# Performance work log

Hardware: AMD Instinct MI355X
Metric: run time of the kernel (lower is better)

The kernel has to match this reference:

```python
import jax, jax.numpy as jnp
import numpy as np

D_MODEL = 256; D_STATE = 128; EXPAND = 2; HEADDIM = 64
D_INNER = EXPAND * D_MODEL            # 512
NHEADS = D_INNER // HEADDIM           # 8
CONV_DIM = D_INNER + 2 * D_STATE      # 768
D_IN_PROJ = 2 * D_INNER + 2 * D_STATE + NHEADS  # 1288
KCONV = 4
BATCH = 16; SEQ = 1024; CHUNK = 64
EPS = 1e-5


def setup_inputs() -> dict:
    key = jax.random.key(0)
    ks = jax.random.split(key, 8)
    # dt_bias = inverse-softplus of dt ~ U[1e-3, 1e-1] (Mamba2 init)
    dt = jnp.exp(jax.random.uniform(ks[3], (NHEADS,), jnp.float32,
                                    np.log(1e-3), np.log(1e-1)))
    dt_bias = dt + jnp.log(-jnp.expm1(-dt))
    return {
        "u": jax.random.normal(ks[0], (BATCH, SEQ, D_MODEL), jnp.float32),
        "W_in": 0.02 * jax.random.normal(ks[1], (D_MODEL, D_IN_PROJ), jnp.float32),
        "conv_w": 0.2 * jax.random.normal(ks[2], (CONV_DIM, KCONV), jnp.float32),
        "conv_b": jnp.zeros((CONV_DIM,), jnp.float32),
        "dt_bias": dt_bias,
        "A_log": jnp.log(jax.random.uniform(ks[4], (NHEADS,), jnp.float32, 1.0, 16.0)),
        "D": jnp.ones((NHEADS,), jnp.float32),
        "norm_w": jnp.ones((D_INNER,), jnp.float32),
        "W_out": 0.02 * jax.random.normal(ks[5], (D_INNER, D_MODEL), jnp.float32),
    }


def _segsum(x):
    # x: (..., L) -> (..., L, L) lower-triangular cumulative segment sums
    L = x.shape[-1]
    c = jnp.cumsum(x, axis=-1)
    ss = c[..., :, None] - c[..., None, :]
    mask = jnp.tril(jnp.ones((L, L), bool))
    return jnp.where(mask, ss, -jnp.inf)


def _ssd(X, A, Bm, Cm, chunk):
    # Chunked SSD selective scan (Mamba2, ngroups=1).
    # X:(b,t,h,p)  A:(b,t,h)  Bm,Cm:(b,t,n)
    b, t, h, p = X.shape
    nc = t // chunk
    X = X.reshape(b, nc, chunk, h, p)
    A = A.reshape(b, nc, chunk, h).transpose(0, 3, 1, 2)   # (b,h,c,l)
    Bm = Bm.reshape(b, nc, chunk, -1)
    Cm = Cm.reshape(b, nc, chunk, -1)
    A_cs = jnp.cumsum(A, axis=-1)                          # (b,h,c,l)
    Lmat = jnp.exp(_segsum(A))                             # (b,h,c,l,l)
    # within-chunk (diagonal) contribution
    Y_diag = jnp.einsum('bcln,bcsn,bhcls,bcshp->bclhp', Cm, Bm, Lmat, X)
    # per-chunk end states
    decay_states = jnp.exp(A_cs[..., -1:] - A_cs)          # (b,h,c,l)
    states = jnp.einsum('bcln,bhcl,bclhp->bchpn', Bm, decay_states, X)
    # inter-chunk recurrence (vectorized over chunks)
    A_chunk = jnp.pad(A_cs[..., -1], ((0, 0), (0, 0), (1, 0)))
    decay_chunk = jnp.exp(_segsum(A_chunk))                # (b,h,c+1,c+1)
    states = jnp.concatenate([jnp.zeros_like(states[:, :1]), states], axis=1)
    new_states = jnp.einsum('bhzc,bchpn->bzhpn', decay_chunk, states)
    states = new_states[:, :-1]                            # state entering each chunk
    Y_off = jnp.einsum('bcln,bchpn,bhcl->bclhp', Cm, states, jnp.exp(A_cs))
    return (Y_diag + Y_off).reshape(b, t, h, p)


def reference(u, W_in, conv_w, conv_b, dt_bias, A_log, D, norm_w, W_out):
    B, T, _ = u.shape
    zxbcdt = u @ W_in                                      # (B,T,1288)
    z, xBC, dt = jnp.split(zxbcdt, [D_INNER, D_INNER + CONV_DIM], axis=-1)
    # causal depthwise conv1d, kernel KCONV
    xp = jnp.pad(xBC, ((0, 0), (KCONV - 1, 0), (0, 0)))
    kern = conv_w.T[:, None, :]                            # (K,1,C)
    xBC = jax.lax.conv_general_dilated(
        xp, kern, (1,), 'VALID',
        dimension_numbers=('NWC', 'WIO', 'NWC'), feature_group_count=CONV_DIM)
    xBC = jax.nn.silu(xBC + conv_b)
    x, Bc, Cc = jnp.split(xBC, [D_INNER, D_INNER + D_STATE], axis=-1)
    x = x.reshape(B, T, NHEADS, HEADDIM)
    dt = jax.nn.softplus(dt + dt_bias)                     # (B,T,H)
    A = -jnp.exp(A_log)                                    # (H,)
    y = _ssd(x * dt[..., None], dt * A, Bc, Cc, CHUNK)     # (B,T,H,P)
    y = y + D[:, None] * x                                 # skip term
    y = y.reshape(B, T, D_INNER)
    # gated RMSNorm: norm(y * silu(z)) * weight
    g = y * jax.nn.silu(z)
    g = g * jax.lax.rsqrt(jnp.mean(g * g, axis=-1, keepdims=True) + EPS) * norm_w
    return g @ W_out
```

## Files before the change

kernel.cpp:

```cpp
#include <hip/hip_runtime.h>
#include <hip/hip_bf16.h>
#include <math.h>

#define BATCHN  16
#define SEQ     1024
#define DMODEL  256
#define DSTATE  128
#define HEADDIM 64
#define DINNER  512
#define NHEADS  8
#define CONVDIM 768
#define DINPROJ 1288
#define ZXLD    1280
#define KCONV   4
#define NCHUNK  16
#define LCHUNK  64
#define EPSV    1e-5f
#define ROWS    (BATCHN*SEQ)

typedef __attribute__((ext_vector_type(8))) __bf16 bf16x8;
typedef __attribute__((ext_vector_type(4))) float  f32x4;

__device__ inline ushort f2bf(float f) {
    union { float f; uint32_t u; } v; v.f = f;
    uint32_t r = v.u + 0x7fff + ((v.u >> 16) & 1);
    return (ushort)(r >> 16);
}
__device__ inline float bf2f(ushort u) {
    union { uint32_t u; float f; } v; v.u = ((uint32_t)u) << 16;
    return v.f;
}

__global__ __launch_bounds__(256) void cast_bf16_k(const float* __restrict__ src,
                                                   ushort* __restrict__ dst) {
    const int idx = blockIdx.x * 256 + threadIdx.x;
    float4 a = *(const float4*)&src[(size_t)idx * 8];
    float4 b = *(const float4*)&src[(size_t)idx * 8 + 4];
    ushort r[8];
    r[0]=f2bf(a.x); r[1]=f2bf(a.y); r[2]=f2bf(a.z); r[3]=f2bf(a.w);
    r[4]=f2bf(b.x); r[5]=f2bf(b.y); r[6]=f2bf(b.z); r[7]=f2bf(b.w);
    *(uint4*)&dst[(size_t)idx * 8] = *(uint4*)r;
}

__global__ __launch_bounds__(256) void transpose_cast_k(const float* __restrict__ src,
                                                        ushort* __restrict__ dst,
                                                        int K, int ldsrc, int col0) {
    __shared__ float Ts[32][33];
    const int tx = threadIdx.x & 31, ty = threadIdx.x >> 5;
    const int n0 = blockIdx.x * 32, k0 = blockIdx.y * 32;
    #pragma unroll
    for (int j = 0; j < 4; ++j) {
        int kl = ty * 4 + j;
        Ts[kl][tx] = src[(size_t)(k0 + kl) * ldsrc + col0 + n0 + tx];
    }
    __syncthreads();
    #pragma unroll
    for (int j = 0; j < 4; ++j) {
        int nl = ty * 4 + j;
        dst[(size_t)(n0 + nl) * K + k0 + tx] = f2bf(Ts[tx][nl]);
    }
}

#define LDSW 72
template<typename CT>
__global__ __launch_bounds__(256) void gemm_bf16(const ushort* __restrict__ A,
                                                 const ushort* __restrict__ Bt,
                                                 CT* __restrict__ C,
                                                 int M, int N, int K, int nx) {
    __shared__ ushort As[128 * LDSW];
    __shared__ ushort Bs[128 * LDSW];
    const int tid  = threadIdx.x;
    const int nwg  = gridDim.x;
    const int work = (blockIdx.x & 7) * (nwg >> 3) + (blockIdx.x >> 3);
    const int m0 = (work / nx) * 128, n0 = (work % nx) * 128;
    const int wid = tid >> 6, lane = tid & 63;
    const int wr = wid >> 1, wc = wid & 1;
    const int r = tid >> 1, kq = tid & 1;
    const int fr = lane & 15, kc = lane >> 4;

    f32x4 acc[4][4];
    #pragma unroll
    for (int i = 0; i < 4; ++i)
        #pragma unroll
        for (int j = 0; j < 4; ++j) acc[i][j] = (f32x4)0.f;

    for (int kt = 0; kt < K; kt += 64) {
        const ushort* ap = &A [(size_t)(m0 + r) * K + kt + kq * 32];
        const ushort* bp = &Bt[(size_t)(n0 + r) * K + kt + kq * 32];
        #pragma unroll
        for (int v = 0; v < 4; ++v) {
            *(uint4*)&As[r * LDSW + kq * 32 + v * 8] = *(const uint4*)(ap + v * 8);
            *(uint4*)&Bs[r * LDSW + kq * 32 + v * 8] = *(const uint4*)(bp + v * 8);
        }
        __syncthreads();
        #pragma unroll
        for (int kk = 0; kk < 2; ++kk) {
            bf16x8 af[4], bfv[4];
            #pragma unroll
            for (int i = 0; i < 4; ++i) {
                af[i]  = *(const bf16x8*)&As[(wr * 64 + i * 16 + fr) * LDSW + kk * 32 + kc * 8];
                bfv[i] = *(const bf16x8*)&Bs[(wc * 64 + i * 16 + fr) * LDSW + kk * 32 + kc * 8];
            }
            #pragma unroll
            for (int i = 0; i < 4; ++i)
                #pragma unroll
                for (int j = 0; j < 4; ++j)
                    acc[i][j] = __builtin_amdgcn_mfma_f32_16x16x32_bf16(af[i], bfv[j], acc[i][j], 0, 0, 0);
        }
        __syncthreads();
    }
    #pragma unroll
    for (int i = 0; i < 4; ++i)
        #pragma unroll
        for (int j = 0; j < 4; ++j)
            #pragma unroll
            for (int q = 0; q < 4; ++q) {
                int rr = m0 + wr * 64 + i * 16 + (lane >> 4) * 4 + q;
                int cc = n0 + wc * 64 + j * 16 + (lane & 15);
                if constexpr (sizeof(CT) == 4) C[(size_t)rr * N + cc] = acc[i][j][q];
                else                           C[(size_t)rr * N + cc] = f2bf(acc[i][j][q]);
            }
}

__global__ __launch_bounds__(256) void dt_fused_k(const float* __restrict__ u,
                                                  const float* __restrict__ W_in,
                                                  const float* __restrict__ dt_bias,
                                                  const float* __restrict__ A_log,
                                                  float* __restrict__ dtb,
                                                  float* __restrict__ adtb) {
    __shared__ float Ws[DMODEL][NHEADS];
    const int tid = threadIdx.x;
    #pragma unroll
    for (int j = 0; j < 8; ++j) {
        int idx = tid + j * 256;
        Ws[idx >> 3][idx & 7] = W_in[(size_t)(idx >> 3) * DINPROJ + 1280 + (idx & 7)];
    }
    __syncthreads();
    const int lane = tid & 63, w = tid >> 6;
    const int h = lane & 7;
    const int row = blockIdx.x * 32 + w * 8 + (lane >> 3);
    const float* up = &u[(size_t)row * DMODEL];
    float acc = 0.f;
    for (int k = 0; k < DMODEL; k += 4) {
        float4 uv = *(const float4*)(up + k);
        acc += uv.x * Ws[k][h] + uv.y * Ws[k+1][h] + uv.z * Ws[k+2][h] + uv.w * Ws[k+3][h];
    }
    float v = acc + dt_bias[h];
    float dt = (v > 20.f) ? v : log1pf(__expf(v));
    dtb [(size_t)row * NHEADS + h] = dt;
    adtb[(size_t)row * NHEADS + h] = dt * (-__expf(A_log[h]));
}

__global__ __launch_bounds__(256) void conv_silu_k(const ushort* __restrict__ zx,
                                                   const float* __restrict__ cw,
                                                   const float* __restrict__ cb,
                                                   ushort* __restrict__ out) {
    __shared__ float cws[KCONV][CONVDIM];
    __shared__ float cbs[CONVDIM];
    const int tid = threadIdx.x;
    #pragma unroll
    for (int it = 0; it < 3; ++it) {
        int i = tid + it * 256;
        cbs[i] = cb[i];
        #pragma unroll
        for (int k = 0; k < KCONV; ++k) cws[k][i] = cw[i * KCONV + k];
    }
    __syncthreads();

    const int idx = blockIdx.x * 256 + tid;
    const int cg = idx % 96, btq = idx / 96;
    const int c0 = cg * 8;
    const int bt0 = btq * 4;
    const int t0 = bt0 & (SEQ - 1);

    float wv[KCONV][8], bias[8];
    #pragma unroll
    for (int j = 0; j < 8; ++j) bias[j] = cbs[c0 + j];
    #pragma unroll
    for (int k = 0; k < KCONV; ++k) {
        float4 a = *(const float4*)&cws[k][c0];
        float4 b = *(const float4*)&cws[k][c0 + 4];
        wv[k][0] = a.x; wv[k][1] = a.y; wv[k][2] = a.z; wv[k][3] = a.w;
        wv[k][4] = b.x; wv[k][5] = b.y; wv[k][6] = b.z; wv[k][7] = b.w;
    }
    float xr[7][8];
    #pragma unroll
    for (int r = 0; r < 7; ++r) {
        int tt = t0 - 3 + r;
        if (tt >= 0) {
            uint4 v = *(const uint4*)&zx[(size_t)(bt0 - 3 + r) * ZXLD + DINNER + c0];
            const ushort* pv = (const ushort*)&v;
            #pragma unroll
            for (int j = 0; j < 8; ++j) xr[r][j] = bf2f(pv[j]);
        } else {
            #pragma unroll
            for (int j = 0; j < 8; ++j) xr[r][j] = 0.f;
        }
    }
    #pragma unroll
    for (int dt = 0; dt < 4; ++dt) {
        float acc[8];
        #pragma unroll
        for (int j = 0; j < 8; ++j) acc[j] = bias[j];
        #pragma unroll
        for (int k = 0; k < KCONV; ++k)
            #pragma unroll
            for (int j = 0; j < 8; ++j) acc[j] += xr[dt + k][j] * wv[k][j];
        ushort res[8];
        #pragma unroll
        for (int j = 0; j < 8; ++j)
            res[j] = f2bf(acc[j] / (1.f + __expf(-acc[j])));
        *(uint4*)&out[(size_t)(bt0 + dt) * CONVDIM + c0] = *(uint4*)res;
    }
}

#define SLDA 136
#define SLDB 72
__global__ __launch_bounds__(256) void ssd_mfma_k(const ushort* __restrict__ xbc,
                                                  const float* __restrict__ dtb,
                                                  const float* __restrict__ adtb,
                                                  const float* __restrict__ Dp,
                                                  ushort* __restrict__ ybuf,
                                                  ushort* __restrict__ states,
                                                  float* __restrict__ acsbuf,
                                                  float* __restrict__ chunksum) {
    const int c = blockIdx.x, b = blockIdx.y, hgrp = blockIdx.z;
    const int row0 = b * SEQ + c * LCHUNK;
    const int tid = threadIdx.x;
    const int lane = tid & 63, w = tid >> 6;
    const int fr = lane & 15, kc = lane >> 4;

    __shared__ union {
        struct { ushort Bs[64][SLDA]; ushort Cs[64][SLDA]; } p1;
        struct { ushort Ps[64][SLDB]; ushort Xt[64][SLDB]; ushort Xdt[64][SLDB]; } p2;
    } U;
    __shared__ ushort Btr[128][SLDB];
    __shared__ float acs4[4][64];
    __shared__ float dts[4][64];

    {
        const int hh = hgrp * 4 + w;
        float v = adtb[(size_t)(row0 + lane) * NHEADS + hh];
        #pragma unroll
        for (int off = 1; off < 64; off <<= 1) {
            float t = __shfl_up(v, off);
            if (lane >= off) v += t;
        }
        acs4[w][lane] = v;
        acsbuf[(((size_t)b * NCHUNK + c) * NHEADS + hh) * LCHUNK + lane] = v;
        if (lane == 63) chunksum[((size_t)b * NCHUNK + c) * NHEADS + hh] = v;
        dts[w][lane] = dtb[(size_t)(row0 + lane) * NHEADS + hh];
    }
    for (int it = 0; it < 4; ++it) {
        int idx = tid + it * 256;
        int l = idx >> 4, ng = idx & 15;
        const ushort* rp = &xbc[(size_t)(row0 + l) * CONVDIM + DINNER];
        uint4 vb = *(const uint4*)(rp + ng * 8);
        *(uint4*)&U.p1.Bs[l][ng * 8] = vb;
        uint4 vc = *(const uint4*)(rp + DSTATE + ng * 8);
        *(uint4*)&U.p1.Cs[l][ng * 8] = vc;
        const ushort* pv = (const ushort*)&vb;
        #pragma unroll
        for (int j = 0; j < 8; ++j) Btr[ng * 8 + j][l] = pv[j];
    }
    __syncthreads();

    const int wr = w >> 1, wc = w & 1;
    f32x4 accG[2][2];
    #pragma unroll
    for (int i = 0; i < 2; ++i)
        #pragma unroll
        for (int j = 0; j < 2; ++j) accG[i][j] = (f32x4)0.f;
    #pragma unroll
    for (int kt = 0; kt < 4; ++kt) {
        bf16x8 af[2], bfv[2];
        #pragma unroll
        for (int i = 0; i < 2; ++i) af[i]  = *(const bf16x8*)&U.p1.Cs[wr*32 + i*16 + fr][kt*32 + kc*8];
        #pragma unroll
        for (int j = 0; j < 2; ++j) bfv[j] = *(const bf16x8*)&U.p1.Bs[wc*32 + j*16 + fr][kt*32 + kc*8];
        #pragma unroll
        for (int i = 0; i < 2; ++i)
            #pragma unroll
            for (int j = 0; j < 2; ++j)
                accG[i][j] = __builtin_amdgcn_mfma_f32_16x16x32_bf16(af[i], bfv[j], accG[i][j], 0, 0, 0);
    }
    __syncthreads();

    for (int hl = 0; hl < 4; ++hl) {
        const int hh = hgrp * 4 + hl;
        const float acsL = acs4[hl][63];
        const float dec_l = __expf(acsL - acs4[hl][lane]);
        const float dt_l  = dts[hl][lane];
        #pragma unroll
        for (int i = 0; i < 4; ++i) {
            int p0 = w * 16 + i * 4;
            ushort4 xv = *(const ushort4*)&xbc[(size_t)(row0 + lane) * CONVDIM + hh * HEADDIM + p0];
            float x0 = bf2f(xv.x) * dt_l, x1 = bf2f(xv.y) * dt_l;
            float x2 = bf2f(xv.z) * dt_l, x3 = bf2f(xv.w) * dt_l;
            U.p2.Xt [p0+0][lane] = f2bf(x0); U.p2.Xdt[p0+0][lane] = f2bf(x0 * dec_l);
            U.p2.Xt [p0+1][lane] = f2bf(x1); U.p2.Xdt[p0+1][lane] = f2bf(x1 * dec_l);
            U.p2.Xt [p0+2][lane] = f2bf(x2); U.p2.Xdt[p0+2][lane] = f2bf(x2 * dec_l);
            U.p2.Xt [p0+3][lane] = f2bf(x3); U.p2.Xdt[p0+3][lane] = f2bf(x3 * dec_l);
        }
        #pragma unroll
        for (int i = 0; i < 2; ++i)
            #pragma unroll
            for (int j = 0; j < 2; ++j)
                #pragma unroll
                for (int q = 0; q < 4; ++q) {
                    int l = wr*32 + i*16 + (lane >> 4)*4 + q;
                    int s = wc*32 + j*16 + fr;
                    float v = 0.f;
                    if (s < l)       v = accG[i][j][q] * __expf(acs4[hl][l] - acs4[hl][s]);
                    else if (s == l) v = accG[i][j][q] + Dp[hh] / dts[hl][l];
                    U.p2.Ps[l][s] = f2bf(v);
                }
        __syncthreads();
        {
            f32x4 acc[4];
            #pragma unroll
            for (int j = 0; j < 4; ++j) acc[j] = (f32x4)0.f;
            #pragma unroll
            for (int kt = 0; kt < 2; ++kt) {
                bf16x8 af = *(const bf16x8*)&U.p2.Ps[w*16 + fr][kt*32 + kc*8];
                #pragma unroll
                for (int j = 0; j < 4; ++j) {
                    bf16x8 bfv = *(const bf16x8*)&U.p2.Xt[j*16 + fr][kt*32 + kc*8];
                    acc[j] = __builtin_amdgcn_mfma_f32_16x16x32_bf16(af, bfv, acc[j], 0, 0, 0);
                }
            }
            #pragma unroll
            for (int j = 0; j < 4; ++j)
                #pragma unroll
                for (int q = 0; q < 4; ++q) {
                    int l = w*16 + (lane >> 4)*4 + q;
                    int p = j*16 + fr;
                    ybuf[(size_t)(row0 + l) * DINNER + hh * HEADDIM + p] = f2bf(acc[j][q]);
                }
        }
        {
            f32x4 acc2[4][2];
            #pragma unroll
            for (int mt = 0; mt < 4; ++mt)
                #pragma unroll
                for (int jt = 0; jt < 2; ++jt) acc2[mt][jt] = (f32x4)0.f;
            #pragma unroll
            for (int kt = 0; kt < 2; ++kt) {
                bf16x8 a4[4], b2[2];
                #pragma unroll
                for (int mt = 0; mt < 4; ++mt) a4[mt] = *(const bf16x8*)&U.p2.Xdt[mt*16 + fr][kt*32 + kc*8];
                #pragma unroll
                for (int jt = 0; jt < 2; ++jt) b2[jt] = *(const bf16x8*)&Btr[w*32 + jt*16 + fr][kt*32 + kc*8];
                #pragma unroll
                for (int mt = 0; mt < 4; ++mt)
                    #pragma unroll
                    for (int jt = 0; jt < 2; ++jt)
                        acc2[mt][jt] = __builtin_amdgcn_mfma_f32_16x16x32_bf16(a4[mt], b2[jt], acc2[mt][jt], 0, 0, 0);
            }
            ushort* sb = states + ((((size_t)b * NCHUNK + c) * NHEADS + hh) * HEADDIM) * DSTATE;
            #pragma unroll
            for (int mt = 0; mt < 4; ++mt)
                #pragma unroll
                for (int jt = 0; jt < 2; ++jt)
                    #pragma unroll
                    for (int q = 0; q < 4; ++q) {
                        int p = mt*16 + (lane >> 4)*4 + q;
                        int n = w*32 + jt*16 + fr;
                        sb[(size_t)p * DSTATE + n] = f2bf(acc2[mt][jt][q]);
                    }
        }
        __syncthreads();
    }
}

__global__ __launch_bounds__(256) void scan_k(ushort* __restrict__ states,
                                              const float* __restrict__ chunksum) {
    const int bid = blockIdx.x;
    const int pq = bid & 3, h = (bid >> 2) & 7, b = bid >> 5;
    const int tid = threadIdx.x;
    float pref[8];
    #pragma unroll
    for (int k = 0; k < 8; ++k) pref[k] = 0.f;
    for (int c = 0; c < NCHUNK; ++c) {
        ushort* base = states + (((size_t)b * NCHUNK + c) * NHEADS + h) * (HEADDIM * DSTATE)
                       + pq * 2048 + tid * 8;
        float dec = __expf(chunksum[((size_t)b * NCHUNK + c) * NHEADS + h]);
        uint4 v = *(const uint4*)base;
        const ushort* pv = (const ushort*)&v;
        ushort outv[8];
        #pragma unroll
        for (int j = 0; j < 8; ++j) {
            float cur = bf2f(pv[j]);
            outv[j] = f2bf(pref[j]);
            pref[j] = dec * pref[j] + cur;
        }
        *(uint4*)base = *(uint4*)outv;
    }
}

#define YLDS 520
__global__ __launch_bounds__(256) void yoff_gate_k(const ushort* __restrict__ xbc,
                                                   const ushort* __restrict__ states,
                                                   const float* __restrict__ acsbuf,
                                                   const ushort* __restrict__ ybuf,
                                                   const ushort* __restrict__ zx,
                                                   const float* __restrict__ nw,
                                                   ushort* __restrict__ gbuf) {
    const int c = blockIdx.x, b = blockIdx.y;
    const int row0 = b * SEQ + c * LCHUNK;
    const int tid = threadIdx.x;
    const int lane = tid & 63, w = tid >> 6;
    const int fr = lane & 15, kc = lane >> 4;
    __shared__ ushort Csh[64][SLDA];
    __shared__ ushort Ssh[64][SLDA];
    __shared__ ushort Ys[64][YLDS];
    __shared__ float eah[64];

    for (int it = 0; it < 4; ++it) {
        int idx = tid + it * 256;
        int l = idx >> 4, ng = idx & 15;
        *(uint4*)&Csh[l][ng * 8] =
            *(const uint4*)&xbc[(size_t)(row0 + l) * CONVDIM + DINNER + DSTATE + ng * 8];
    }
    for (int hl = 0; hl < NHEADS; ++hl) {
        __syncthreads();
        const ushort* sb = states + ((((size_t)b * NCHUNK + c) * NHEADS + hl) * HEADDIM) * DSTATE;
        for (int it = 0; it < 4; ++it) {
            int idx = tid + it * 256;
            int p = idx >> 4, ng = idx & 15;
            *(uint4*)&Ssh[p][ng * 8] = *(const uint4*)&sb[(size_t)p * DSTATE + ng * 8];
        }
        if (tid < 64)
            eah[tid] = __expf(acsbuf[(((size_t)b * NCHUNK + c) * NHEADS + hl) * LCHUNK + tid]);
        __syncthreads();
        f32x4 acc[4];
        #pragma unroll
        for (int j = 0; j < 4; ++j) acc[j] = (f32x4)0.f;
        #pragma unroll
        for (int kt = 0; kt < 4; ++kt) {
            bf16x8 af = *(const bf16x8*)&Csh[w*16 + fr][kt*32 + kc*8];
            #pragma unroll
            for (int j = 0; j < 4; ++j) {
                bf16x8 bfv = *(const bf16x8*)&Ssh[j*16 + fr][kt*32 + kc*8];
                acc[j] = __builtin_amdgcn_mfma_f32_16x16x32_bf16(af, bfv, acc[j], 0, 0, 0);
            }
        }
        #pragma unroll
        for (int j = 0; j < 4; ++j)
            #pragma unroll
            for (int q = 0; q < 4; ++q) {
                int l = w*16 + (lane >> 4)*4 + q;
                int p = j*16 + fr;
                float val = bf2f(ybuf[(size_t)(row0 + l) * DINNER + hl * HEADDIM + p])
                            + acc[j][q] * eah[l];
                Ys[l][hl * HEADDIM + p] = f2bf(val);
            }
    }
    __syncthreads();
    float nwv[8];
    #pragma unroll
    for (int j = 0; j < 8; ++j) nwv[j] = nw[lane * 8 + j];
    for (int i = 0; i < 16; ++i) {
        int l = w * 16 + i;
        int row = row0 + l;
        uint4 zv = *(const uint4*)&zx[(size_t)row * ZXLD + lane * 8];
        const ushort* pz = (const ushort*)&zv;
        float g[8], ss = 0.f;
        #pragma unroll
        for (int j = 0; j < 8; ++j) {
            float y = bf2f(Ys[l][lane * 8 + j]);
            float z = bf2f(pz[j]);
            float sz = z / (1.f + __expf(-z));
            g[j] = y * sz;
            ss += g[j] * g[j];
        }
        #pragma unroll
        for (int off = 32; off; off >>= 1) ss += __shfl_xor(ss, off);
        float r = rsqrtf(ss / (float)DINNER + EPSV);
        ushort res[8];
        #pragma unroll
        for (int j = 0; j < 8; ++j) res[j] = f2bf(g[j] * r * nwv[j]);
        *(uint4*)&gbuf[(size_t)row * DINNER + lane * 8] = *(uint4*)res;
    }
}

extern "C" void kernel_launch(void* const* d_in, const int* in_sizes, int n_in,
                              void* d_out, int out_size, void* d_ws, size_t ws_size,
                              hipStream_t stream) {
    const float* u       = (const float*)d_in[0];
    const float* W_in    = (const float*)d_in[1];
    const float* conv_w  = (const float*)d_in[2];
    const float* conv_b  = (const float*)d_in[3];
    const float* dt_bias = (const float*)d_in[4];
    const float* A_log   = (const float*)d_in[5];
    const float* Dp      = (const float*)d_in[6];
    const float* norm_w  = (const float*)d_in[7];
    const float* W_out   = (const float*)d_in[8];
    float* out = (float*)d_out;

    char* p = (char*)d_ws;
    ushort* zx       = (ushort*)p; p += (size_t)ROWS * ZXLD * sizeof(ushort);
    ushort* ybuf     = (ushort*)p; p += (size_t)ROWS * DINNER * sizeof(ushort);
    ushort* gbuf     = (ushort*)p; p += (size_t)ROWS * DINNER * sizeof(ushort);
    ushort* states   = (ushort*)p; p += (size_t)BATCHN * NCHUNK * NHEADS * HEADDIM * DSTATE * sizeof(ushort);
    ushort* xbc      = (ushort*)p; p += (size_t)ROWS * CONVDIM * sizeof(ushort);
    ushort* ubf      = (ushort*)p; p += (size_t)ROWS * DMODEL * sizeof(ushort);
    float*  dtb      = (float*)p;  p += (size_t)ROWS * NHEADS  * sizeof(float);
    float*  adtb     = (float*)p;  p += (size_t)ROWS * NHEADS  * sizeof(float);
    float*  chunksum = (float*)p;  p += (size_t)BATCHN * NCHUNK * NHEADS * sizeof(float);
    float*  acsbuf   = (float*)p;  p += (size_t)BATCHN * NCHUNK * NHEADS * LCHUNK * sizeof(float);
    ushort* WtA      = (ushort*)p; p += (size_t)ZXLD * DMODEL * sizeof(ushort);
    ushort* WtB      = (ushort*)p; p += (size_t)DMODEL * DINNER * sizeof(ushort);

    transpose_cast_k<<<dim3(ZXLD/32, DMODEL/32), 256, 0, stream>>>(W_in,  WtA, DMODEL, DINPROJ, 0);
    transpose_cast_k<<<dim3(DMODEL/32, DINNER/32), 256, 0, stream>>>(W_out, WtB, DINNER, DMODEL, 0);
    cast_bf16_k<<<ROWS*DMODEL/8/256, 256, 0, stream>>>(u, ubf);
    gemm_bf16<ushort><<<(ZXLD/128)*(ROWS/128), 256, 0, stream>>>(
        ubf, WtA, zx, ROWS, ZXLD, DMODEL, ZXLD/128);
    dt_fused_k<<<ROWS/32, 256, 0, stream>>>(u, W_in, dt_bias, A_log, dtb, adtb);
    conv_silu_k<<<(ROWS/4)*96/256, 256, 0, stream>>>(zx, conv_w, conv_b, xbc);
    ssd_mfma_k<<<dim3(NCHUNK, BATCHN, 2), 256, 0, stream>>>(
        xbc, dtb, adtb, Dp, ybuf, states, acsbuf, chunksum);
    scan_k<<<BATCHN*NHEADS*4, 256, 0, stream>>>(states, chunksum);
    yoff_gate_k<<<dim3(NCHUNK, BATCHN), 256, 0, stream>>>(
        xbc, states, acsbuf, ybuf, zx, norm_w, gbuf);
    gemm_bf16<float><<<(DMODEL/128)*(ROWS/128), 256, 0, stream>>>(
        gbuf, WtB, out, ROWS, DMODEL, DINNER, DMODEL/128);
}
```

Baseline: 139.6 us.

## Fuse u cast with dt projection, merge weight transposes, and restructure SSD X staging

Combines the u-to-bf16 cast with the dt projection so u is read once and staged in shared memory, and merges the two weight transpose-cast launches into one grid. This cuts two kernel launches and one full read of u. In the SSD kernel, the per-row decay factor is precomputed once into shared memory, and the X transposed tiles are built with lanes indexing headdim and packed 4-wide stores. That replaces scalar strided LDS writes, at the cost of scalar global loads of xbc.

```diff
diff --git a/kernel.cpp b/kernel.cpp
--- a/kernel.cpp
+++ b/kernel.cpp
@@ -31,27 +31,21 @@
     return v.f;
 }
 
-__global__ __launch_bounds__(256) void cast_bf16_k(const float* __restrict__ src,
-                                                   ushort* __restrict__ dst) {
-    const int idx = blockIdx.x * 256 + threadIdx.x;
-    float4 a = *(const float4*)&src[(size_t)idx * 8];
-    float4 b = *(const float4*)&src[(size_t)idx * 8 + 4];
-    ushort r[8];
-    r[0]=f2bf(a.x); r[1]=f2bf(a.y); r[2]=f2bf(a.z); r[3]=f2bf(a.w);
-    r[4]=f2bf(b.x); r[5]=f2bf(b.y); r[6]=f2bf(b.z); r[7]=f2bf(b.w);
-    *(uint4*)&dst[(size_t)idx * 8] = *(uint4*)r;
-}
-
-__global__ __launch_bounds__(256) void transpose_cast_k(const float* __restrict__ src,
-                                                        ushort* __restrict__ dst,
-                                                        int K, int ldsrc, int col0) {
+__global__ __launch_bounds__(256) void transpose_cast2_k(const float* __restrict__ W_in,
+                                                         const float* __restrict__ W_out,
+                                                         ushort* __restrict__ WtA,
+                                                         ushort* __restrict__ WtB) {
     __shared__ float Ts[32][33];
+    int bid = blockIdx.x;
+    const float* src; ushort* dst; int K, ldsrc, nx;
+    if (bid < 320) { src = W_in;  dst = WtA; K = DMODEL; ldsrc = DINPROJ; nx = 40; }
+    else { bid -= 320; src = W_out; dst = WtB; K = DINNER; ldsrc = DMODEL; nx = 8; }
+    const int n0 = (bid % nx) * 32, k0 = (bid / nx) * 32;
     const int tx = threadIdx.x & 31, ty = threadIdx.x >> 5;
-    const int n0 = blockIdx.x * 32, k0 = blockIdx.y * 32;
     #pragma unroll
     for (int j = 0; j < 4; ++j) {
         int kl = ty * 4 + j;
-        Ts[kl][tx] = src[(size_t)(k0 + kl) * ldsrc + col0 + n0 + tx];
+        Ts[kl][tx] = src[(size_t)(k0 + kl) * ldsrc + n0 + tx];
     }
     __syncthreads();
     #pragma unroll
@@ -59,6 +53,46 @@
         int nl = ty * 4 + j;
         dst[(size_t)(n0 + nl) * K + k0 + tx] = f2bf(Ts[tx][nl]);
     }
+}
+
+__global__ __launch_bounds__(256) void dt_cast_k(const float* __restrict__ u,
+                                                 const float* __restrict__ W_in,
+                                                 const float* __restrict__ dt_bias,
+                                                 const float* __restrict__ A_log,
+                                                 ushort* __restrict__ ubf,
+                                                 float* __restrict__ dtb,
+                                                 float* __restrict__ adtb) {
+    __shared__ float Uld[32][264];
+    __shared__ float Ws[DMODEL][NHEADS];
+    const int tid = threadIdx.x;
+    #pragma unroll
+    for (int j = 0; j < 8; ++j) {
+        int idx = tid + j * 256;
+        Ws[idx >> 3][idx & 7] = W_in[(size_t)(idx >> 3) * DINPROJ + 1280 + (idx & 7)];
+    }
+    const int row0 = blockIdx.x * 32;
+    #pragma unroll
+    for (int v = 0; v < 8; ++v) {
+        int e = v * 1024 + tid * 4;
+        int r = e >> 8, cc = e & 255;
+        float4 x = *(const float4*)&u[(size_t)(row0 + r) * DMODEL + cc];
+        *(float4*)&Uld[r][cc] = x;
+        ushort t4[4];
+        t4[0]=f2bf(x.x); t4[1]=f2bf(x.y); t4[2]=f2bf(x.z); t4[3]=f2bf(x.w);
+        *(ushort4*)&ubf[(size_t)(row0 + r) * DMODEL + cc] = *(ushort4*)t4;
+    }
+    __syncthreads();
+    const int row = tid >> 3, h = tid & 7;
+    float acc = 0.f;
+    #pragma unroll 8
+    for (int k = 0; k < DMODEL; k += 4) {
+        float4 uv = *(const float4*)&Uld[row][k];
+        acc += uv.x * Ws[k][h] + uv.y * Ws[k+1][h] + uv.z * Ws[k+2][h] + uv.w * Ws[k+3][h];
+    }
+    float v = acc + dt_bias[h];
+    float dt = (v > 20.f) ? v : log1pf(__expf(v));
+    dtb [(size_t)(row0 + row) * NHEADS + h] = dt;
+    adtb[(size_t)(row0 + row) * NHEADS + h] = dt * (-__expf(A_log[h]));
 }
 
 #define LDSW 72
@@ -122,35 +156,6 @@
             }
 }
 
-__global__ __launch_bounds__(256) void dt_fused_k(const float* __restrict__ u,
-                                                  const float* __restrict__ W_in,
-                                                  const float* __restrict__ dt_bias,
-                                                  const float* __restrict__ A_log,
-                                                  float* __restrict__ dtb,
-                                                  float* __restrict__ adtb) {
-    __shared__ float Ws[DMODEL][NHEADS];
-    const int tid = threadIdx.x;
-    #pragma unroll
-    for (int j = 0; j < 8; ++j) {
-        int idx = tid + j * 256;
-        Ws[idx >> 3][idx & 7] = W_in[(size_t)(idx >> 3) * DINPROJ + 1280 + (idx & 7)];
-    }
-    __syncthreads();
-    const int lane = tid & 63, w = tid >> 6;
-    const int h = lane & 7;
-    const int row = blockIdx.x * 32 + w * 8 + (lane >> 3);
-    const float* up = &u[(size_t)row * DMODEL];
-    float acc = 0.f;
-    for (int k = 0; k < DMODEL; k += 4) {
-        float4 uv = *(const float4*)(up + k);
-        acc += uv.x * Ws[k][h] + uv.y * Ws[k+1][h] + uv.z * Ws[k+2][h] + uv.w * Ws[k+3][h];
-    }
-    float v = acc + dt_bias[h];
-    float dt = (v > 20.f) ? v : log1pf(__expf(v));
-    dtb [(size_t)row * NHEADS + h] = dt;
-    adtb[(size_t)row * NHEADS + h] = dt * (-__expf(A_log[h]));
-}
-
 __global__ __launch_bounds__(256) void conv_silu_k(const ushort* __restrict__ zx,
                                                    const float* __restrict__ cw,
                                                    const float* __restrict__ cb,
@@ -237,6 +242,7 @@
     __shared__ ushort Btr[128][SLDB];
     __shared__ float acs4[4][64];
     __shared__ float dts[4][64];
+    __shared__ float decs[4][64];
 
     {
         const int hh = hgrp * 4 + w;
@@ -247,6 +253,8 @@
             if (lane >= off) v += t;
         }
         acs4[w][lane] = v;
+        float tot = __shfl(v, 63);
+        decs[w][lane] = __expf(tot - v);
         acsbuf[(((size_t)b * NCHUNK + c) * NHEADS + hh) * LCHUNK + lane] = v;
         if (lane == 63) chunksum[((size_t)b * NCHUNK + c) * NHEADS + hh] = v;
         dts[w][lane] = dtb[(size_t)(row0 + lane) * NHEADS + hh];
@@ -288,19 +296,22 @@
 
     for (int hl = 0; hl < 4; ++hl) {
         const int hh = hgrp * 4 + hl;
-        const float acsL = acs4[hl][63];
-        const float dec_l = __expf(acsL - acs4[hl][lane]);
-        const float dt_l  = dts[hl][lane];
-        #pragma unroll
-        for (int i = 0; i < 4; ++i) {
-            int p0 = w * 16 + i * 4;
-            ushort4 xv = *(const ushort4*)&xbc[(size_t)(row0 + lane) * CONVDIM + hh * HEADDIM + p0];
-            float x0 = bf2f(xv.x) * dt_l, x1 = bf2f(xv.y) * dt_l;
-            float x2 = bf2f(xv.z) * dt_l, x3 = bf2f(xv.w) * dt_l;
-            U.p2.Xt [p0+0][lane] = f2bf(x0); U.p2.Xdt[p0+0][lane] = f2bf(x0 * dec_l);
-            U.p2.Xt [p0+1][lane] = f2bf(x1); U.p2.Xdt[p0+1][lane] = f2bf(x1 * dec_l);
-            U.p2.Xt [p0+2][lane] = f2bf(x2); U.p2.Xdt[p0+2][lane] = f2bf(x2 * dec_l);
-            U.p2.Xt [p0+3][lane] = f2bf(x3); U.p2.Xdt[p0+3][lane] = f2bf(x3 * dec_l);
+        {
+            const int p = lane;
+            ushort xt[16], xdt[16];
+            #pragma unroll
+            for (int j = 0; j < 16; ++j) {
+                int l = w * 16 + j;
+                float xv = bf2f(xbc[(size_t)(row0 + l) * CONVDIM + hh * HEADDIM + p])
+                           * dts[hl][l];
+                xt[j]  = f2bf(xv);
+                xdt[j] = f2bf(xv * decs[hl][l]);
+            }
+            #pragma unroll
+            for (int v = 0; v < 4; ++v) {
+                *(ushort4*)&U.p2.Xt [p][w*16 + v*4] = *(ushort4*)&xt[v*4];
+                *(ushort4*)&U.p2.Xdt[p][w*16 + v*4] = *(ushort4*)&xdt[v*4];
+            }
         }
         #pragma unroll
         for (int i = 0; i < 2; ++i)
@@ -512,12 +523,10 @@
     ushort* WtA      = (ushort*)p; p += (size_t)ZXLD * DMODEL * sizeof(ushort);
     ushort* WtB      = (ushort*)p; p += (size_t)DMODEL * DINNER * sizeof(ushort);
 
-    transpose_cast_k<<<dim3(ZXLD/32, DMODEL/32), 256, 0, stream>>>(W_in,  WtA, DMODEL, DINPROJ, 0);
-    transpose_cast_k<<<dim3(DMODEL/32, DINNER/32), 256, 0, stream>>>(W_out, WtB, DINNER, DMODEL, 0);
-    cast_bf16_k<<<ROWS*DMODEL/8/256, 256, 0, stream>>>(u, ubf);
+    dt_cast_k<<<ROWS/32, 256, 0, stream>>>(u, W_in, dt_bias, A_log, ubf, dtb, adtb);
+    transpose_cast2_k<<<448, 256, 0, stream>>>(W_in, W_out, WtA, WtB);
     gemm_bf16<ushort><<<(ZXLD/128)*(ROWS/128), 256, 0, stream>>>(
         ubf, WtA, zx, ROWS, ZXLD, DMODEL, ZXLD/128);
-    dt_fused_k<<<ROWS/32, 256, 0, stream>>>(u, W_in, dt_bias, A_log, dtb, adtb);
     conv_silu_k<<<(ROWS/4)*96/256, 256, 0, stream>>>(zx, conv_w, conv_b, xbc);
     ssd_mfma_k<<<dim3(NCHUNK, BATCHN, 2), 256, 0, stream>>>(
         xbc, dtb, adtb, Dp, ybuf, states, acsbuf, chunksum);
```

Measured after the change: 131.4 us. 1.06x faster.
